# Optimization experiments

Measured on AMD Instinct MI355X. Metric: run time of the kernel, lower is better.

Reference implementation:

```python
import jax, jax.numpy as jnp
import numpy as np

N = 8192          # number of samples (atoms)
D_IN = 256        # in_features (descriptor dim)
D_OUT = 256       # out_features
NUM_TYPE = 64     # number of atom types
INIT_VAL = 0.01


def setup_inputs() -> dict:
    key = jax.random.key(0)
    k1, k2, k3, k4 = jax.random.split(key, 4)
    batch_i = jax.random.randint(k1, (N,), 0, NUM_TYPE)                     # [N] type index per sample
    batch_descriptor = jax.random.normal(k2, (N, D_IN), dtype=jnp.float32)  # [N, D_IN]
    layer1 = INIT_VAL * jax.random.normal(k3, (NUM_TYPE, D_OUT, D_IN), dtype=jnp.float32)
    W = INIT_VAL * jax.random.normal(k4, (D_OUT, D_IN), dtype=jnp.float32)  # linear_adjust.weight
    b = jnp.zeros((D_OUT,), dtype=jnp.float32)                              # linear_adjust.bias (init 0)
    return {"batch_i": batch_i, "batch_descriptor": batch_descriptor,
            "layer1": layer1, "W": W, "b": b}


def reference(batch_i, batch_descriptor, layer1, W, b):
    # Per-sample type-indexed weight gather + batched mat-vec (torch.bmm)
    # layer1[batch_i]: [N, D_OUT, D_IN]; descriptor: [N, D_IN] -> [N, D_OUT]
    gathered = layer1[batch_i]
    out = jnp.einsum('noi,ni->no', gathered, batch_descriptor)
    out = jnp.tanh(out)  # ACT assumed tanh (undefined in snippet)
    # linear_adjust: x @ W.T + b
    adjust = batch_descriptor @ W.T + b
    return out + adjust
```

## Files before the change

kernel.cpp:

```cpp
#include <hip/hip_runtime.h>
#include <cstddef>

#define NUM_TYPE 64
#define DD 256
#define NN 8192
#define GM64 192
#define LSTR 40

typedef __bf16 bf16x8 __attribute__((ext_vector_type(8)));
typedef __bf16 bf16x4 __attribute__((ext_vector_type(4)));
typedef float f32x4 __attribute__((ext_vector_type(4)));

__device__ __forceinline__ bf16x4 cvt4(float4 v) {
  bf16x4 h;
  h[0] = (__bf16)v.x; h[1] = (__bf16)v.y; h[2] = (__bf16)v.z; h[3] = (__bf16)v.w;
  return h;
}

__device__ __forceinline__ float tanh_fast(float x) {
  float xc = fminf(fmaxf(x, -15.f), 15.f);
  float e = __expf(2.f * xc);
  return (e - 1.f) / (e + 1.f);
}

__global__ __launch_bounds__(1024) void build_perm64(
    const int* __restrict__ bi, int* __restrict__ type_off,
    int* __restrict__ perm, int* __restrict__ gtype, int* __restrict__ gfirst) {
  __shared__ int wcnt[16][NUM_TYPE];
  __shared__ int wbase[16][NUM_TYPE];
  __shared__ int cnt[NUM_TYPE];
  __shared__ int tstart[NUM_TYPE];
  __shared__ int gbase[NUM_TYPE];
  __shared__ int totals[2];
  const int tid = threadIdx.x;
  const int w = tid >> 6;
  for (int i = tid; i < 16 * NUM_TYPE; i += 1024) ((int*)wcnt)[i] = 0;
  __syncthreads();
  int myv[8];
#pragma unroll
  for (int rnd = 0; rnd < 8; ++rnd) {
    int v = bi[rnd * 1024 + tid];
    myv[rnd] = v;
    atomicAdd(&wcnt[w][v], 1);
  }
  __syncthreads();
  if (tid < NUM_TYPE) {
    int s = 0;
#pragma unroll
    for (int ww = 0; ww < 16; ++ww) { wbase[ww][tid] = s; s += wcnt[ww][tid]; }
    cnt[tid] = s;
  }
  __syncthreads();
  if (tid == 0) {
    int s = 0, p = 0;
    for (int t = 0; t < NUM_TYPE; ++t) {
      tstart[t] = s; gbase[t] = p;
      s += cnt[t];
      p += (cnt[t] + 63) >> 6;
    }
    totals[0] = s; totals[1] = p;
  }
  __syncthreads();
  if (tid < NUM_TYPE) {
    const int c = cnt[tid];
    const int ngr = (c + 63) >> 6;
    const int g0 = gbase[tid];
    const int s0 = tstart[tid];
    for (int j = 0; j < ngr; ++j) { gtype[g0 + j] = tid; gfirst[g0 + j] = s0 + j * 64; }
    type_off[tid] = s0;
#pragma unroll
    for (int ww = 0; ww < 16; ++ww) wbase[ww][tid] += s0;
  }
  if (tid == 0) type_off[NUM_TYPE] = totals[0];
  for (int g = totals[1] + tid; g < GM64; g += 1024) gtype[g] = -1;
  __syncthreads();
#pragma unroll
  for (int rnd = 0; rnd < 8; ++rnd) {
    int v = myv[rnd];
    int p = atomicAdd(&wbase[w][v], 1);
    perm[p] = rnd * 1024 + tid;
  }
}

__global__ __launch_bounds__(256) void gemm_tile(
    const float* __restrict__ desc,
    const float* __restrict__ layer1,
    const float* __restrict__ W,
    const float* __restrict__ bias,
    const int* __restrict__ type_off,
    const int* __restrict__ perm,
    const int* __restrict__ gtype,
    const int* __restrict__ gfirst,
    float* __restrict__ out) {
  const int d = blockIdx.x;
  const int l = (d & 7) * 96 + (d >> 3);
  const int g = l >> 2;
  const int cb = l & 3;
  const int t = gtype[g];
  if (t < 0) return;
  const int first = gfirst[g];
  const int limit = type_off[t + 1];

  const int tid = threadIdx.x;
  const int w = tid >> 6;
  const int lane = tid & 63;
  const int l15 = lane & 15;
  const int lg = lane >> 4;
  const int wr = w >> 1;
  const int wc = w & 1;

  __shared__ __bf16 At[2][64][LSTR];
  __shared__ __bf16 Bl[2][64][LSTR];
  __shared__ __bf16 Bw[2][64][LSTR];

  const int srow = tid >> 2;
  const int fseg = tid & 3;
  const int ar = first + srow;
  const int sA = (ar < limit) ? perm[ar] : -1;
  const float* aP  = desc + (size_t)(sA < 0 ? 0 : sA) * DD + fseg * 8;
  const int gcol = cb * 64 + srow;
  const float* blP = layer1 + ((size_t)t * DD + gcol) * DD + fseg * 8;
  const float* bwP = W + (size_t)gcol * DD + fseg * 8;

#define STAGE(buf, kb)                                                        \
  {                                                                           \
    float4 a0 = make_float4(0.f,0.f,0.f,0.f), a1 = a0;                        \
    if (sA >= 0) {                                                            \
      a0 = *reinterpret_cast<const float4*>(aP + (kb));                       \
      a1 = *reinterpret_cast<const float4*>(aP + (kb) + 4);                   \
    }                                                                         \
    float4 b0 = *reinterpret_cast<const float4*>(blP + (kb));                 \
    float4 b1 = *reinterpret_cast<const float4*>(blP + (kb) + 4);             \
    float4 w0 = *reinterpret_cast<const float4*>(bwP + (kb));                 \
    float4 w1 = *reinterpret_cast<const float4*>(bwP + (kb) + 4);             \
    *reinterpret_cast<bf16x4*>(&At[buf][srow][fseg * 8])     = cvt4(a0);      \
    *reinterpret_cast<bf16x4*>(&At[buf][srow][fseg * 8 + 4]) = cvt4(a1);      \
    *reinterpret_cast<bf16x4*>(&Bl[buf][srow][fseg * 8])     = cvt4(b0);      \
    *reinterpret_cast<bf16x4*>(&Bl[buf][srow][fseg * 8 + 4]) = cvt4(b1);      \
    *reinterpret_cast<bf16x4*>(&Bw[buf][srow][fseg * 8])     = cvt4(w0);      \
    *reinterpret_cast<bf16x4*>(&Bw[buf][srow][fseg * 8 + 4]) = cvt4(w1);      \
  }

  STAGE(0, 0)
  __syncthreads();

  f32x4 accL[2][2] = {};
  f32x4 accW[2][2] = {};
  int buf = 0;
#pragma unroll
  for (int kc = 0; kc < 8; ++kc) {
    if (kc < 7) STAGE(buf ^ 1, (kc + 1) * 32)
    bf16x8 af[2], bl[2], bw[2];
#pragma unroll
    for (int m = 0; m < 2; ++m)
      af[m] = *reinterpret_cast<const bf16x8*>(&At[buf][wr * 32 + m * 16 + l15][lg * 8]);
#pragma unroll
    for (int n = 0; n < 2; ++n) {
      bl[n] = *reinterpret_cast<const bf16x8*>(&Bl[buf][wc * 32 + n * 16 + l15][lg * 8]);
      bw[n] = *reinterpret_cast<const bf16x8*>(&Bw[buf][wc * 32 + n * 16 + l15][lg * 8]);
    }
#pragma unroll
    for (int m = 0; m < 2; ++m)
#pragma unroll
      for (int n = 0; n < 2; ++n) {
        accL[m][n] = __builtin_amdgcn_mfma_f32_16x16x32_bf16(af[m], bl[n], accL[m][n], 0, 0, 0);
        accW[m][n] = __builtin_amdgcn_mfma_f32_16x16x32_bf16(af[m], bw[n], accW[m][n], 0, 0, 0);
      }
    __syncthreads();
    buf ^= 1;
  }
#undef STAGE

#pragma unroll
  for (int m = 0; m < 2; ++m) {
    const int orow = first + wr * 32 + m * 16 + l15;
    const int sOut = (orow < limit) ? perm[orow] : -1;
#pragma unroll
    for (int i = 0; i < 4; ++i) {
      const int sv = __shfl(sOut, lg * 4 + i, 64);
      if (sv >= 0) {
        float* op = out + (size_t)sv * DD + cb * 64 + wc * 32 + l15;
#pragma unroll
        for (int n = 0; n < 2; ++n) {
          const float bv = bias[cb * 64 + wc * 32 + n * 16 + l15];
          __builtin_nontemporal_store(tanh_fast(accL[m][n][i]) + accW[m][n][i] + bv,
                                      op + n * 16);
        }
      }
    }
  }
}

extern "C" void kernel_launch(void* const* d_in, const int* in_sizes, int n_in,
                              void* d_out, int out_size, void* d_ws, size_t ws_size,
                              hipStream_t stream) {
  const int* bi       = (const int*)d_in[0];
  const float* desc   = (const float*)d_in[1];
  const float* layer1 = (const float*)d_in[2];
  const float* W      = (const float*)d_in[3];
  const float* bias   = (const float*)d_in[4];
  float* out = (float*)d_out;

  char* ws = (char*)d_ws;
  int* type_off = (int*)(ws);
  int* gtype    = (int*)(ws + 1024);
  int* gfirst   = (int*)(ws + 4096);
  int* perm     = (int*)(ws + 8192);

  hipLaunchKernelGGL(build_perm64, dim3(1), dim3(1024), 0, stream,
                     bi, type_off, perm, gtype, gfirst);
  hipLaunchKernelGGL(gemm_tile, dim3(GM64 * 4), dim3(256), 0, stream,
                     desc, layer1, W, bias, type_off, perm, gtype, gfirst, out);
}
```

Baseline: 25.76 us.

## Pre-convert inputs to bf16 and pre-gather permuted descriptors in a prep kernel

Adds a prep kernel that converts layer1 and W to bf16 and writes the descriptor rows, gathered in permuted group order, as bf16 into workspace. The GEMM kernel then loads contiguous bf16x8 vectors straight into shared memory, with no fp32-to-bf16 conversion and no indirect row gather. In exchange the whole 16MB layer1 tensor is read and rewritten every call, including types that no group uses, and an extra kernel launch is added.

```diff
diff --git a/kernel.cpp b/kernel.cpp
--- a/kernel.cpp
+++ b/kernel.cpp
@@ -82,10 +82,60 @@
   }
 }
 
-__global__ __launch_bounds__(256) void gemm_tile(
+__global__ __launch_bounds__(256) void prep_kernel(
     const float* __restrict__ desc,
     const float* __restrict__ layer1,
     const float* __restrict__ W,
+    const int* __restrict__ type_off,
+    const int* __restrict__ perm,
+    const int* __restrict__ gtype,
+    const int* __restrict__ gfirst,
+    __bf16* __restrict__ Lp,
+    __bf16* __restrict__ Wp,
+    __bf16* __restrict__ Ap) {
+  const int b = blockIdx.x;
+  const int tid = threadIdx.x;
+  if (b < 512) {
+    const float4* src = reinterpret_cast<const float4*>(layer1);
+#pragma unroll
+    for (int it = 0; it < 8; ++it) {
+      const int idx = b * 2048 + it * 256 + tid;
+      *reinterpret_cast<bf16x4*>(Lp + (size_t)idx * 4) = cvt4(src[idx]);
+    }
+  } else if (b < 528) {
+    const float4* src = reinterpret_cast<const float4*>(W);
+#pragma unroll
+    for (int it = 0; it < 4; ++it) {
+      const int idx = (b - 512) * 1024 + it * 256 + tid;
+      *reinterpret_cast<bf16x4*>(Wp + (size_t)idx * 4) = cvt4(src[idx]);
+    }
+  } else {
+    const int bb = b - 528;
+    const int lane = tid & 63;
+    const int wv = tid >> 6;
+#pragma unroll
+    for (int it = 0; it < 12; ++it) {
+      const int slot = bb * 48 + it * 4 + wv;
+      const int g = slot >> 6;
+      const int j = slot & 63;
+      const int t = gtype[g];
+      int src = -1;
+      if (t >= 0) {
+        const int r = gfirst[g] + j;
+        if (r < type_off[t + 1]) src = perm[r];
+      }
+      bf16x4 h = {};
+      if (src >= 0)
+        h = cvt4(reinterpret_cast<const float4*>(desc + (size_t)src * DD)[lane]);
+      *reinterpret_cast<bf16x4*>(Ap + (size_t)slot * DD + lane * 4) = h;
+    }
+  }
+}
+
+__global__ __launch_bounds__(256) void gemm_tile(
+    const __bf16* __restrict__ Ap,
+    const __bf16* __restrict__ Lp,
+    const __bf16* __restrict__ Wp,
     const float* __restrict__ bias,
     const int* __restrict__ type_off,
     const int* __restrict__ perm,
@@ -114,31 +164,20 @@
   __shared__ __bf16 Bw[2][64][LSTR];
 
   const int srow = tid >> 2;
-  const int fseg = tid & 3;
-  const int ar = first + srow;
-  const int sA = (ar < limit) ? perm[ar] : -1;
-  const float* aP  = desc + (size_t)(sA < 0 ? 0 : sA) * DD + fseg * 8;
+  const int seg = tid & 3;
+  const __bf16* aP  = Ap + ((size_t)g * 64 + srow) * DD + seg * 8;
   const int gcol = cb * 64 + srow;
-  const float* blP = layer1 + ((size_t)t * DD + gcol) * DD + fseg * 8;
-  const float* bwP = W + (size_t)gcol * DD + fseg * 8;
+  const __bf16* blP = Lp + ((size_t)t * DD + gcol) * DD + seg * 8;
+  const __bf16* bwP = Wp + (size_t)gcol * DD + seg * 8;
 
 #define STAGE(buf, kb)                                                        \
   {                                                                           \
-    float4 a0 = make_float4(0.f,0.f,0.f,0.f), a1 = a0;                        \
-    if (sA >= 0) {                                                            \
-      a0 = *reinterpret_cast<const float4*>(aP + (kb));                       \
-      a1 = *reinterpret_cast<const float4*>(aP + (kb) + 4);                   \
-    }                                                                         \
-    float4 b0 = *reinterpret_cast<const float4*>(blP + (kb));                 \
-    float4 b1 = *reinterpret_cast<const float4*>(blP + (kb) + 4);             \
-    float4 w0 = *reinterpret_cast<const float4*>(bwP + (kb));                 \
-    float4 w1 = *reinterpret_cast<const float4*>(bwP + (kb) + 4);             \
-    *reinterpret_cast<bf16x4*>(&At[buf][srow][fseg * 8])     = cvt4(a0);      \
-    *reinterpret_cast<bf16x4*>(&At[buf][srow][fseg * 8 + 4]) = cvt4(a1);      \
-    *reinterpret_cast<bf16x4*>(&Bl[buf][srow][fseg * 8])     = cvt4(b0);      \
-    *reinterpret_cast<bf16x4*>(&Bl[buf][srow][fseg * 8 + 4]) = cvt4(b1);      \
-    *reinterpret_cast<bf16x4*>(&Bw[buf][srow][fseg * 8])     = cvt4(w0);      \
-    *reinterpret_cast<bf16x4*>(&Bw[buf][srow][fseg * 8 + 4]) = cvt4(w1);      \
+    *reinterpret_cast<bf16x8*>(&At[buf][srow][seg * 8]) =                     \
+        *reinterpret_cast<const bf16x8*>(aP + (kb));                          \
+    *reinterpret_cast<bf16x8*>(&Bl[buf][srow][seg * 8]) =                     \
+        *reinterpret_cast<const bf16x8*>(blP + (kb));                         \
+    *reinterpret_cast<bf16x8*>(&Bw[buf][srow][seg * 8]) =                     \
+        *reinterpret_cast<const bf16x8*>(bwP + (kb));                         \
   }
 
   STAGE(0, 0)
@@ -206,9 +245,14 @@
   int* gtype    = (int*)(ws + 1024);
   int* gfirst   = (int*)(ws + 4096);
   int* perm     = (int*)(ws + 8192);
+  __bf16* Ap    = (__bf16*)(ws + 65536);
+  __bf16* Lp    = (__bf16*)(ws + 65536 + 6291456);
+  __bf16* Wp    = (__bf16*)(ws + 65536 + 6291456 + 8388608);
 
   hipLaunchKernelGGL(build_perm64, dim3(1), dim3(1024), 0, stream,
                      bi, type_off, perm, gtype, gfirst);
+  hipLaunchKernelGGL(prep_kernel, dim3(784), dim3(256), 0, stream,
+                     desc, layer1, W, type_off, perm, gtype, gfirst, Lp, Wp, Ap);
   hipLaunchKernelGGL(gemm_tile, dim3(GM64 * 4), dim3(256), 0, stream,
-                     desc, layer1, W, bias, type_off, perm, gtype, gfirst, out);
-}
+                     Ap, Lp, Wp, bias, type_off, perm, gtype, gfirst, out);
+}
```

Measured after the change: 37.54 us. +45.8%, slower.
